# Optimization experiments

Hardware: AMD Instinct MI355X
Metric: run time of the kernel (lower is better)

Reference implementation:

```python
import jax, jax.numpy as jnp
import numpy as np

N_NODES = 100000
N_EDGES = 1600000
N_FEAT, N_HID, N_CLS = 256, 64, 16


def setup_inputs() -> dict:
    key = jax.random.key(0)
    ks = jax.random.split(key, 8)
    x = jax.random.normal(ks[0], (N_NODES, N_FEAT), dtype=jnp.float32)
    adj_row = jax.random.randint(ks[1], (N_EDGES,), 0, N_NODES, dtype=jnp.int32)
    adj_col = jax.random.randint(ks[2], (N_EDGES,), 0, N_NODES, dtype=jnp.int32)
    adj_vals = jax.random.uniform(ks[3], (N_EDGES,), dtype=jnp.float32)
    W1 = jax.random.normal(ks[4], (N_FEAT, N_HID), dtype=jnp.float32) * 0.05
    b1 = jnp.zeros((N_HID,), dtype=jnp.float32)
    W2 = jax.random.normal(ks[5], (N_HID, N_CLS), dtype=jnp.float32) * 0.05
    b2 = jnp.zeros((N_CLS,), dtype=jnp.float32)
    return {"x": x, "adj_row": adj_row, "adj_col": adj_col, "adj_vals": adj_vals,
            "W1": W1, "b1": b1, "W2": W2, "b2": b2}


def _spmm(row, col, vals, h):
    # sparse [N,N] @ dense [N,D]: gather source rows, scale, scatter-add to dest rows
    msgs = vals[:, None] * h[col]                       # [E, D]
    return jax.ops.segment_sum(msgs, row, num_segments=N_NODES)


def reference(x, adj_row, adj_col, adj_vals, W1, b1, W2, b2):
    # layer 1: linear -> spmm -> relu  (dropout is identity at inference)
    h = _spmm(adj_row, adj_col, adj_vals, x @ W1 + b1)  # [N, n_hidden]
    h = jax.nn.relu(h)
    # layer 2: linear -> spmm -> log_softmax
    out = _spmm(adj_row, adj_col, adj_vals, h @ W2 + b2)  # [N, n_class]
    return jax.nn.log_softmax(out, axis=1)
```

## Files before the change

### kernel.cpp

```cpp
#include <hip/hip_runtime.h>

#define N_NODES 100000
#define N_EDGES 1600000
#define N_FEAT  256
#define N_HID   64
#define N_CLS   16
#define NB      391
#define CHUNK   8192
#define NSCAT   196
#define NGEMM1  1563
#define NHIST   256

typedef unsigned short bfraw;
typedef unsigned int uint32;

typedef __attribute__((ext_vector_type(8))) short  bf16x8;
typedef __attribute__((ext_vector_type(4))) float  f32x4;

__device__ __forceinline__ bfraw f2bf(float f) {
    union { float f; unsigned int i; } v; v.f = f;
    unsigned int x = v.i;
    return (bfraw)((x + 0x7FFFu + ((x >> 16) & 1u)) >> 16);
}

__device__ __forceinline__ float bf_lo(uint32 g) { return __uint_as_float(g << 16); }
__device__ __forceinline__ float bf_hi(uint32 g) { return __uint_as_float(g & 0xFFFF0000u); }

__global__ __launch_bounds__(256) void w1cvt_hist_k(const float* __restrict__ W1,
                                                    bfraw* __restrict__ w1f,
                                                    const int* __restrict__ rowi,
                                                    int* __restrict__ part) {
    __shared__ int lh[NB];
    if (blockIdx.x < 64) {
        int i = blockIdx.x * 256 + threadIdx.x;
        int k = i >> 6, n = i & 63;
        w1f[((size_t)((k >> 3) * 64 + n) << 3) + (k & 7)] = f2bf(W1[i]);
        return;
    }
    const int hb = blockIdx.x - 64;
    for (int i = threadIdx.x; i < NB; i += 256) lh[i] = 0;
    __syncthreads();
    const int4* r4p = (const int4*)rowi;
    for (int i = hb * 256 + threadIdx.x; i < N_EDGES / 4; i += 256 * 256) {
        int4 r = r4p[i];
        atomicAdd(&lh[r.x >> 8], 1);
        atomicAdd(&lh[r.y >> 8], 1);
        atomicAdd(&lh[r.z >> 8], 1);
        atomicAdd(&lh[r.w >> 8], 1);
    }
    __syncthreads();
    for (int i = threadIdx.x; i < NB; i += 256)
        part[hb * NB + i] = lh[i];
}

__global__ __launch_bounds__(512) void bscan_k(const int* __restrict__ part,
                                               int* __restrict__ bbase,
                                               int* __restrict__ gcur,
                                               int* __restrict__ rp) {
    __shared__ int s[512];
    int t = threadIdx.x;
    int v = 0;
    if (t < NB) {
        #pragma unroll 8
        for (int hb = 0; hb < NHIST; ++hb) v += part[hb * NB + t];
    }
    s[t] = v;
    __syncthreads();
    #pragma unroll
    for (int off = 1; off < 512; off <<= 1) {
        int x = (t >= off) ? s[t - off] : 0;
        __syncthreads();
        s[t] += x;
        __syncthreads();
    }
    if (t <= NB) {
        int b = s[t] - v;
        bbase[t] = b;
        if (t < NB) gcur[t] = b;
    }
    if (t == 0) rp[N_NODES] = N_EDGES;
}

__global__ __launch_bounds__(256) void scatter_gemm1_k(const int* __restrict__ rowi,
                                                       const int* __restrict__ coli,
                                                       const float* __restrict__ vals,
                                                       int* __restrict__ gcur,
                                                       int2* __restrict__ edges,
                                                       const float* __restrict__ x,
                                                       const bfraw* __restrict__ w1f,
                                                       const float* __restrict__ b1,
                                                       bfraw* __restrict__ h0) {
    __shared__ int lh[NB];
    __shared__ int lb[NB];
    const int t = threadIdx.x;

    if (blockIdx.x < NSCAT) {
        const int e0   = blockIdx.x * CHUNK;
        const bool full = (e0 + CHUNK <= N_EDGES);
        for (int i = t; i < NB; i += 256) lh[i] = 0;
        __syncthreads();

        int4 r4[8];
        if (full) {
            const int4* rp4 = (const int4*)(rowi + e0);
            #pragma unroll
            for (int u = 0; u < 8; ++u) r4[u] = rp4[t + u * 256];
            #pragma unroll
            for (int u = 0; u < 8; ++u) {
                atomicAdd(&lh[r4[u].x >> 8], 1);
                atomicAdd(&lh[r4[u].y >> 8], 1);
                atomicAdd(&lh[r4[u].z >> 8], 1);
                atomicAdd(&lh[r4[u].w >> 8], 1);
            }
        } else {
            for (int j = t; j < CHUNK; j += 256) {
                int e = e0 + j;
                if (e < N_EDGES) atomicAdd(&lh[rowi[e] >> 8], 1);
            }
        }
        __syncthreads();
        for (int i = t; i < NB; i += 256) {
            int c = lh[i];
            lb[i] = c ? atomicAdd(&gcur[i], c) : 0;
            lh[i] = 0;
        }
        __syncthreads();
        if (full) {
            const int4*   cp4 = (const int4*)(coli + e0);
            const float4* vp4 = (const float4*)(vals + e0);
            #pragma unroll
            for (int u = 0; u < 8; ++u) {
                int4   c4 = cp4[t + u * 256];
                float4 v4 = vp4[t + u * 256];
                int r, b, rk;
                r = r4[u].x; b = r >> 8; rk = atomicAdd(&lh[b], 1);
                edges[lb[b] + rk] = make_int2(c4.x | ((r & 255) << 17), __float_as_int(v4.x));
                r = r4[u].y; b = r >> 8; rk = atomicAdd(&lh[b], 1);
                edges[lb[b] + rk] = make_int2(c4.y | ((r & 255) << 17), __float_as_int(v4.y));
                r = r4[u].z; b = r >> 8; rk = atomicAdd(&lh[b], 1);
                edges[lb[b] + rk] = make_int2(c4.z | ((r & 255) << 17), __float_as_int(v4.z));
                r = r4[u].w; b = r >> 8; rk = atomicAdd(&lh[b], 1);
                edges[lb[b] + rk] = make_int2(c4.w | ((r & 255) << 17), __float_as_int(v4.w));
            }
        } else {
            for (int j = t; j < CHUNK; j += 256) {
                int e = e0 + j;
                if (e < N_EDGES) {
                    int r  = rowi[e];
                    int b  = r >> 8;
                    int rk = atomicAdd(&lh[b], 1);
                    edges[lb[b] + rk] = make_int2(coli[e] | ((r & 255) << 17),
                                                  __float_as_int(vals[e]));
                }
            }
        }
        return;
    }

    const int bg   = blockIdx.x - NSCAT;
    const int w    = t >> 6;
    const int lane = t & 63;
    const int q    = lane >> 4;
    const int m    = lane & 15;

    const int row  = bg * 64 + w * 16 + m;
    const int srow = row < N_NODES ? row : N_NODES - 1;
    const float* xp = x + (size_t)srow * N_FEAT + q * 8;
    const bf16x8* w1v = (const bf16x8*)w1f;

    float4 x0[8], x1[8];
    #pragma unroll
    for (int s = 0; s < 8; ++s) {
        x0[s] = *(const float4*)(xp + s * 32);
        x1[s] = *(const float4*)(xp + s * 32 + 4);
    }

    f32x4 acc[4];
    #pragma unroll
    for (int nt = 0; nt < 4; ++nt) acc[nt] = (f32x4){0.f, 0.f, 0.f, 0.f};

    #pragma unroll
    for (int s = 0; s < 8; ++s) {
        bf16x8 af;
        af[0] = (short)f2bf(x0[s].x); af[1] = (short)f2bf(x0[s].y);
        af[2] = (short)f2bf(x0[s].z); af[3] = (short)f2bf(x0[s].w);
        af[4] = (short)f2bf(x1[s].x); af[5] = (short)f2bf(x1[s].y);
        af[6] = (short)f2bf(x1[s].z); af[7] = (short)f2bf(x1[s].w);
        const int g = s * 4 + q;
        #pragma unroll
        for (int nt = 0; nt < 4; ++nt) {
            bf16x8 bf_ = w1v[g * 64 + nt * 16 + m];
            acc[nt] = __builtin_amdgcn_mfma_f32_16x16x32_bf16(af, bf_, acc[nt], 0, 0, 0);
        }
    }

    float bb[4];
    #pragma unroll
    for (int nt = 0; nt < 4; ++nt) bb[nt] = b1[nt * 16 + m];

    const int orow0 = bg * 64 + w * 16 + q * 4;
    #pragma unroll
    for (int r = 0; r < 4; ++r) {
        int orow = orow0 + r;
        if (orow < N_NODES) {
            bfraw* op = h0 + (size_t)orow * N_HID + m;
            #pragma unroll
            for (int nt = 0; nt < 4; ++nt)
                op[nt * 16] = f2bf(acc[nt][r] + bb[nt]);
        }
    }
}

__global__ __launch_bounds__(256) void sort_k(const int* __restrict__ bbase,
                                              const int2* __restrict__ edges,
                                              int2* __restrict__ edges2,
                                              int* __restrict__ rp) {
    __shared__ int cnt[256];
    __shared__ int pos[256];
    const int t   = threadIdx.x;
    const int b   = blockIdx.x;
    const int beg = bbase[b];
    const int end = bbase[b + 1];

    cnt[t] = 0;
    __syncthreads();
    {
        int i = beg + t;
        for (; i + 768 < end; i += 1024) {
            int2 a = edges[i], c = edges[i + 256], d = edges[i + 512], e = edges[i + 768];
            atomicAdd(&cnt[(a.x >> 17) & 255], 1);
            atomicAdd(&cnt[(c.x >> 17) & 255], 1);
            atomicAdd(&cnt[(d.x >> 17) & 255], 1);
            atomicAdd(&cnt[(e.x >> 17) & 255], 1);
        }
        for (; i < end; i += 256)
            atomicAdd(&cnt[(edges[i].x >> 17) & 255], 1);
    }
    __syncthreads();

    int v = cnt[t];
    pos[t] = v;
    __syncthreads();
    #pragma unroll
    for (int off = 1; off < 256; off <<= 1) {
        int y = (t >= off) ? pos[t - off] : 0;
        __syncthreads();
        pos[t] += y;
        __syncthreads();
    }
    int excl = pos[t] - v;

    int row = (b << 8) + t;
    if (row < N_NODES) rp[row] = beg + excl;
    __syncthreads();
    pos[t] = excl;
    __syncthreads();

    {
        int i = beg + t;
        for (; i + 768 < end; i += 1024) {
            int2 E0 = edges[i], E1 = edges[i + 256], E2 = edges[i + 512], E3 = edges[i + 768];
            int r0 = (E0.x >> 17) & 255, r1 = (E1.x >> 17) & 255;
            int r2 = (E2.x >> 17) & 255, r3 = (E3.x >> 17) & 255;
            int k0 = atomicAdd(&pos[r0], 1);
            int k1 = atomicAdd(&pos[r1], 1);
            int k2 = atomicAdd(&pos[r2], 1);
            int k3 = atomicAdd(&pos[r3], 1);
            edges2[beg + k0] = make_int2(E0.x & 0x1FFFF, E0.y);
            edges2[beg + k1] = make_int2(E1.x & 0x1FFFF, E1.y);
            edges2[beg + k2] = make_int2(E2.x & 0x1FFFF, E2.y);
            edges2[beg + k3] = make_int2(E3.x & 0x1FFFF, E3.y);
        }
        for (; i < end; i += 256) {
            int2 E = edges[i];
            int r  = (E.x >> 17) & 255;
            int rk = atomicAdd(&pos[r], 1);
            edges2[beg + rk] = make_int2(E.x & 0x1FFFF, E.y);
        }
    }
}

__global__ __launch_bounds__(256) void spmm1_fused3_k(const int* __restrict__ rp,
                                                      const int2* __restrict__ edges2,
                                                      const uint32* __restrict__ h0p,
                                                      const float* __restrict__ W2,
                                                      const float* __restrict__ b2,
                                                      float* __restrict__ h2) {
    __shared__ float Hs[16][68];
    __shared__ float Ws[64 * 16];
    __shared__ float bs[16];
    const int t = threadIdx.x;
    *(float4*)&Ws[t * 4] = ((const float4*)W2)[t];
    if (t < 16) bs[t] = b2[t];

    const int g16 = t >> 4;
    const int l   = t & 15;
    const int row = blockIdx.x * 16 + g16;
    const int beg = rp[row];
    const int end = rp[row + 1];

    const uint2* h0v = (const uint2*)h0p;

    float a0 = 0.f, a1 = 0.f, a2 = 0.f, a3 = 0.f;
    int i = beg;
    for (; i + 8 <= end; i += 8) {
        int2 E[8];
        #pragma unroll
        for (int u = 0; u < 8; ++u) E[u] = edges2[i + u];
        uint2 q[8];
        #pragma unroll
        for (int u = 0; u < 8; ++u) q[u] = h0v[(size_t)E[u].x * 16 + l];
        #pragma unroll
        for (int u = 0; u < 8; ++u) {
            float v = __int_as_float(E[u].y);
            a0 += v * bf_lo(q[u].x); a1 += v * bf_hi(q[u].x);
            a2 += v * bf_lo(q[u].y); a3 += v * bf_hi(q[u].y);
        }
    }
    for (; i + 4 <= end; i += 4) {
        int2 E[4];
        #pragma unroll
        for (int u = 0; u < 4; ++u) E[u] = edges2[i + u];
        uint2 q[4];
        #pragma unroll
        for (int u = 0; u < 4; ++u) q[u] = h0v[(size_t)E[u].x * 16 + l];
        #pragma unroll
        for (int u = 0; u < 4; ++u) {
            float v = __int_as_float(E[u].y);
            a0 += v * bf_lo(q[u].x); a1 += v * bf_hi(q[u].x);
            a2 += v * bf_lo(q[u].y); a3 += v * bf_hi(q[u].y);
        }
    }
    for (; i < end; ++i) {
        int2 E = edges2[i];
        uint2 q = h0v[(size_t)E.x * 16 + l];
        float v = __int_as_float(E.y);
        a0 += v * bf_lo(q.x); a1 += v * bf_hi(q.x);
        a2 += v * bf_lo(q.y); a3 += v * bf_hi(q.y);
    }

    *(float4*)&Hs[g16][4 * l] = make_float4(fmaxf(a0, 0.f), fmaxf(a1, 0.f),
                                            fmaxf(a2, 0.f), fmaxf(a3, 0.f));
    __syncthreads();

    const int r = t >> 4;
    const int c = t & 15;
    float a = bs[c];
    #pragma unroll
    for (int k = 0; k < 64; ++k)
        a += Hs[r][k] * Ws[k * 16 + c];
    h2[(size_t)(blockIdx.x * 16 + r) * N_CLS + c] = a;
}

__global__ __launch_bounds__(256) void spmm2_lsm_k(const int* __restrict__ rp,
                                                   const int2* __restrict__ edges2,
                                                   const float* __restrict__ h2,
                                                   float* __restrict__ outp) {
    const int l   = threadIdx.x & 7;
    const int row = blockIdx.x * 32 + (threadIdx.x >> 3);
    const int beg = rp[row];
    const int end = rp[row + 1];
    const float2* h2v = (const float2*)h2;

    float a0 = 0.f, a1 = 0.f;
    int i = beg;
    for (; i + 8 <= end; i += 8) {
        int2 e[8];
        #pragma unroll
        for (int u = 0; u < 8; ++u) e[u] = edges2[i + u];
        float2 g[8];
        #pragma unroll
        for (int u = 0; u < 8; ++u) g[u] = h2v[(size_t)e[u].x * 8 + l];
        #pragma unroll
        for (int u = 0; u < 8; ++u) {
            float v = __int_as_float(e[u].y);
            a0 += v * g[u].x; a1 += v * g[u].y;
        }
    }
    for (; i + 4 <= end; i += 4) {
        int2 e[4];
        #pragma unroll
        for (int u = 0; u < 4; ++u) e[u] = edges2[i + u];
        float2 g[4];
        #pragma unroll
        for (int u = 0; u < 4; ++u) g[u] = h2v[(size_t)e[u].x * 8 + l];
        #pragma unroll
        for (int u = 0; u < 4; ++u) {
            float v = __int_as_float(e[u].y);
            a0 += v * g[u].x; a1 += v * g[u].y;
        }
    }
    for (; i < end; ++i) {
        int2 e = edges2[i];
        float2 g = h2v[(size_t)e.x * 8 + l];
        float v = __int_as_float(e.y);
        a0 += v * g.x; a1 += v * g.y;
    }

    float m = fmaxf(a0, a1);
    #pragma unroll
    for (int off = 4; off; off >>= 1) m = fmaxf(m, __shfl_xor(m, off, 8));
    float ex = expf(a0 - m) + expf(a1 - m);
    float s = ex;
    #pragma unroll
    for (int off = 4; off; off >>= 1) s += __shfl_xor(s, off, 8);
    float ls = logf(s);
    *(float2*)(outp + (size_t)row * N_CLS + 2 * l) =
        make_float2(a0 - m - ls, a1 - m - ls);
}

extern "C" void kernel_launch(void* const* d_in, const int* in_sizes, int n_in,
                              void* d_out, int out_size, void* d_ws, size_t ws_size,
                              hipStream_t stream) {
    const float* x        = (const float*)d_in[0];
    const int*   adj_row  = (const int*)d_in[1];
    const int*   adj_col  = (const int*)d_in[2];
    const float* adj_vals = (const float*)d_in[3];
    const float* W1       = (const float*)d_in[4];
    const float* b1       = (const float*)d_in[5];
    const float* W2       = (const float*)d_in[6];
    const float* b2       = (const float*)d_in[7];
    float*       out      = (float*)d_out;

    const size_t H0_BYTES = (size_t)N_NODES * N_HID * sizeof(bfraw);
    const size_t H2_BYTES = (size_t)N_NODES * N_CLS * sizeof(float);
    const size_t E_BYTES  = (size_t)N_EDGES * sizeof(int2);
    bfraw* h0     = (bfraw*)d_ws;
    float* h2     = (float*)((char*)d_ws + H0_BYTES);
    int2*  edges  = (int2*)((char*)h2 + H2_BYTES);
    int2*  edges2 = (int2*)((char*)edges + E_BYTES);
    int*   bbase  = (int*)((char*)edges2 + E_BYTES);
    int*   gcur   = bbase + NB + 1;
    int*   rp     = gcur + NB;
    bfraw* w1f    = (bfraw*)(rp + N_NODES + 1);
    int*   part   = (int*)(w1f + 16384);

    w1cvt_hist_k<<<320, 256, 0, stream>>>(W1, w1f, adj_row, part);
    bscan_k<<<1, 512, 0, stream>>>(part, bbase, gcur, rp);
    scatter_gemm1_k<<<NSCAT + NGEMM1, 256, 0, stream>>>(adj_row, adj_col, adj_vals,
                                                        gcur, edges,
                                                        x, w1f, b1, h0);
    sort_k<<<NB, 256, 0, stream>>>(bbase, edges, edges2, rp);

    spmm1_fused3_k<<<N_NODES / 16, 256, 0, stream>>>(rp, edges2, (const uint32*)h0,
                                                     W2, b2, h2);

    spmm2_lsm_k<<<N_NODES / 32, 256, 0, stream>>>(rp, edges2, h2, out);
}
```

Baseline: 280.6 us.

## Move GEMM1 from scatter kernel into sort kernel and widen scatter blocks

The dense x@W1 GEMM blocks are moved from the scatter launch into the per-bucket sort launch, so GEMM1 runs alongside the sort phase instead of the scatter phase. The scatter becomes its own kernel with 1024-thread blocks, each handling the same 8192-edge chunk with fewer elements per thread. The GEMM inner loop now loads x per step rather than preloading all 16 float4s, which lowers register pressure. The aim is to balance work across the two launches and give better occupancy, at the cost of changing how much overlap each phase gets.

```diff
diff --git a/kernel.cpp b/kernel.cpp
--- a/kernel.cpp
+++ b/kernel.cpp
@@ -81,83 +81,152 @@
     if (t == 0) rp[N_NODES] = N_EDGES;
 }
 
-__global__ __launch_bounds__(256) void scatter_gemm1_k(const int* __restrict__ rowi,
-                                                       const int* __restrict__ coli,
-                                                       const float* __restrict__ vals,
-                                                       int* __restrict__ gcur,
-                                                       int2* __restrict__ edges,
-                                                       const float* __restrict__ x,
-                                                       const bfraw* __restrict__ w1f,
-                                                       const float* __restrict__ b1,
-                                                       bfraw* __restrict__ h0) {
+__global__ __launch_bounds__(1024) void scatter_k(const int* __restrict__ rowi,
+                                                  const int* __restrict__ coli,
+                                                  const float* __restrict__ vals,
+                                                  int* __restrict__ gcur,
+                                                  int2* __restrict__ edges) {
     __shared__ int lh[NB];
     __shared__ int lb[NB];
+    const int t    = threadIdx.x;
+    const int e0   = blockIdx.x * CHUNK;
+    const bool full = (e0 + CHUNK <= N_EDGES);
+    for (int i = t; i < NB; i += 1024) lh[i] = 0;
+    __syncthreads();
+
+    int4 r4[2];
+    if (full) {
+        const int4* rp4 = (const int4*)(rowi + e0);
+        #pragma unroll
+        for (int u = 0; u < 2; ++u) r4[u] = rp4[t + u * 1024];
+        #pragma unroll
+        for (int u = 0; u < 2; ++u) {
+            atomicAdd(&lh[r4[u].x >> 8], 1);
+            atomicAdd(&lh[r4[u].y >> 8], 1);
+            atomicAdd(&lh[r4[u].z >> 8], 1);
+            atomicAdd(&lh[r4[u].w >> 8], 1);
+        }
+    } else {
+        for (int j = t; j < CHUNK; j += 1024) {
+            int e = e0 + j;
+            if (e < N_EDGES) atomicAdd(&lh[rowi[e] >> 8], 1);
+        }
+    }
+    __syncthreads();
+    for (int i = t; i < NB; i += 1024) {
+        int c = lh[i];
+        lb[i] = c ? atomicAdd(&gcur[i], c) : 0;
+        lh[i] = 0;
+    }
+    __syncthreads();
+    if (full) {
+        const int4*   cp4 = (const int4*)(coli + e0);
+        const float4* vp4 = (const float4*)(vals + e0);
+        #pragma unroll
+        for (int u = 0; u < 2; ++u) {
+            int4   c4 = cp4[t + u * 1024];
+            float4 v4 = vp4[t + u * 1024];
+            int r, b, rk;
+            r = r4[u].x; b = r >> 8; rk = atomicAdd(&lh[b], 1);
+            edges[lb[b] + rk] = make_int2(c4.x | ((r & 255) << 17), __float_as_int(v4.x));
+            r = r4[u].y; b = r >> 8; rk = atomicAdd(&lh[b], 1);
+            edges[lb[b] + rk] = make_int2(c4.y | ((r & 255) << 17), __float_as_int(v4.y));
+            r = r4[u].z; b = r >> 8; rk = atomicAdd(&lh[b], 1);
+            edges[lb[b] + rk] = make_int2(c4.z | ((r & 255) << 17), __float_as_int(v4.z));
+            r = r4[u].w; b = r >> 8; rk = atomicAdd(&lh[b], 1);
+            edges[lb[b] + rk] = make_int2(c4.w | ((r & 255) << 17), __float_as_int(v4.w));
+        }
+    } else {
+        for (int j = t; j < CHUNK; j += 1024) {
+            int e = e0 + j;
+            if (e < N_EDGES) {
+                int r  = rowi[e];
+                int b  = r >> 8;
+                int rk = atomicAdd(&lh[b], 1);
+                edges[lb[b] + rk] = make_int2(coli[e] | ((r & 255) << 17),
+                                              __float_as_int(vals[e]));
+            }
+        }
+    }
+}
+
+__global__ __launch_bounds__(256) void sort_gemm1_k(const int* __restrict__ bbase,
+                                                    const int2* __restrict__ edges,
+                                                    int2* __restrict__ edges2,
+                                                    int* __restrict__ rp,
+                                                    const float* __restrict__ x,
+                                                    const bfraw* __restrict__ w1f,
+                                                    const float* __restrict__ b1,
+                                                    bfraw* __restrict__ h0) {
+    __shared__ int cnt[256];
+    __shared__ int pos[256];
     const int t = threadIdx.x;
 
-    if (blockIdx.x < NSCAT) {
-        const int e0   = blockIdx.x * CHUNK;
-        const bool full = (e0 + CHUNK <= N_EDGES);
-        for (int i = t; i < NB; i += 256) lh[i] = 0;
-        __syncthreads();
-
-        int4 r4[8];
-        if (full) {
-            const int4* rp4 = (const int4*)(rowi + e0);
-            #pragma unroll
-            for (int u = 0; u < 8; ++u) r4[u] = rp4[t + u * 256];
-            #pragma unroll
-            for (int u = 0; u < 8; ++u) {
-                atomicAdd(&lh[r4[u].x >> 8], 1);
-                atomicAdd(&lh[r4[u].y >> 8], 1);
-                atomicAdd(&lh[r4[u].z >> 8], 1);
-                atomicAdd(&lh[r4[u].w >> 8], 1);
+    if (blockIdx.x < NB) {
+        const int b   = blockIdx.x;
+        const int beg = bbase[b];
+        const int end = bbase[b + 1];
+
+        cnt[t] = 0;
+        __syncthreads();
+        {
+            int i = beg + t;
+            for (; i + 768 < end; i += 1024) {
+                int2 a = edges[i], c = edges[i + 256], d = edges[i + 512], e = edges[i + 768];
+                atomicAdd(&cnt[(a.x >> 17) & 255], 1);
+                atomicAdd(&cnt[(c.x >> 17) & 255], 1);
+                atomicAdd(&cnt[(d.x >> 17) & 255], 1);
+                atomicAdd(&cnt[(e.x >> 17) & 255], 1);
             }
-        } else {
-            for (int j = t; j < CHUNK; j += 256) {
-                int e = e0 + j;
-                if (e < N_EDGES) atomicAdd(&lh[rowi[e] >> 8], 1);
+            for (; i < end; i += 256)
+                atomicAdd(&cnt[(edges[i].x >> 17) & 255], 1);
+        }
+        __syncthreads();
+
+        int v = cnt[t];
+        pos[t] = v;
+        __syncthreads();
+        #pragma unroll
+        for (int off = 1; off < 256; off <<= 1) {
+            int y = (t >= off) ? pos[t - off] : 0;
+            __syncthreads();
+            pos[t] += y;
+            __syncthreads();
+        }
+        int excl = pos[t] - v;
+
+        int row = (b << 8) + t;
+        if (row < N_NODES) rp[row] = beg + excl;
+        __syncthreads();
+        pos[t] = excl;
+        __syncthreads();
+
+        {
+            int i = beg + t;
+            for (; i + 768 < end; i += 1024) {
+                int2 E0 = edges[i], E1 = edges[i + 256], E2 = edges[i + 512], E3 = edges[i + 768];
+                int r0 = (E0.x >> 17) & 255, r1 = (E1.x >> 17) & 255;
+                int r2 = (E2.x >> 17) & 255, r3 = (E3.x >> 17) & 255;
+                int k0 = atomicAdd(&pos[r0], 1);
+                int k1 = atomicAdd(&pos[r1], 1);
+                int k2 = atomicAdd(&pos[r2], 1);
+                int k3 = atomicAdd(&pos[r3], 1);
+                edges2[beg + k0] = make_int2(E0.x & 0x1FFFF, E0.y);
+                edges2[beg + k1] = make_int2(E1.x & 0x1FFFF, E1.y);
+                edges2[beg + k2] = make_int2(E2.x & 0x1FFFF, E2.y);
+                edges2[beg + k3] = make_int2(E3.x & 0x1FFFF, E3.y);
             }
-        }
-        __syncthreads();
-        for (int i = t; i < NB; i += 256) {
-            int c = lh[i];
-            lb[i] = c ? atomicAdd(&gcur[i], c) : 0;
-            lh[i] = 0;
-        }
-        __syncthreads();
-        if (full) {
-            const int4*   cp4 = (const int4*)(coli + e0);
-            const float4* vp4 = (const float4*)(vals + e0);
-            #pragma unroll
-            for (int u = 0; u < 8; ++u) {
-                int4   c4 = cp4[t + u * 256];
-                float4 v4 = vp4[t + u * 256];
-                int r, b, rk;
-                r = r4[u].x; b = r >> 8; rk = atomicAdd(&lh[b], 1);
-                edges[lb[b] + rk] = make_int2(c4.x | ((r & 255) << 17), __float_as_int(v4.x));
-                r = r4[u].y; b = r >> 8; rk = atomicAdd(&lh[b], 1);
-                edges[lb[b] + rk] = make_int2(c4.y | ((r & 255) << 17), __float_as_int(v4.y));
-                r = r4[u].z; b = r >> 8; rk = atomicAdd(&lh[b], 1);
-                edges[lb[b] + rk] = make_int2(c4.z | ((r & 255) << 17), __float_as_int(v4.z));
-                r = r4[u].w; b = r >> 8; rk = atomicAdd(&lh[b], 1);
-                edges[lb[b] + rk] = make_int2(c4.w | ((r & 255) << 17), __float_as_int(v4.w));
+            for (; i < end; i += 256) {
+                int2 E = edges[i];
+                int r  = (E.x >> 17) & 255;
+                int rk = atomicAdd(&pos[r], 1);
+                edges2[beg + rk] = make_int2(E.x & 0x1FFFF, E.y);
             }
-        } else {
-            for (int j = t; j < CHUNK; j += 256) {
-                int e = e0 + j;
-                if (e < N_EDGES) {
-                    int r  = rowi[e];
-                    int b  = r >> 8;
-                    int rk = atomicAdd(&lh[b], 1);
-                    edges[lb[b] + rk] = make_int2(coli[e] | ((r & 255) << 17),
-                                                  __float_as_int(vals[e]));
-                }
-            }
         }
         return;
     }
 
-    const int bg   = blockIdx.x - NSCAT;
+    const int bg   = blockIdx.x - NB;
     const int w    = t >> 6;
     const int lane = t & 63;
     const int q    = lane >> 4;
@@ -168,24 +237,19 @@
     const float* xp = x + (size_t)srow * N_FEAT + q * 8;
     const bf16x8* w1v = (const bf16x8*)w1f;
 
-    float4 x0[8], x1[8];
+    f32x4 acc[4];
+    #pragma unroll
+    for (int nt = 0; nt < 4; ++nt) acc[nt] = (f32x4){0.f, 0.f, 0.f, 0.f};
+
     #pragma unroll
     for (int s = 0; s < 8; ++s) {
-        x0[s] = *(const float4*)(xp + s * 32);
-        x1[s] = *(const float4*)(xp + s * 32 + 4);
-    }
-
-    f32x4 acc[4];
-    #pragma unroll
-    for (int nt = 0; nt < 4; ++nt) acc[nt] = (f32x4){0.f, 0.f, 0.f, 0.f};
-
-    #pragma unroll
-    for (int s = 0; s < 8; ++s) {
+        float4 a0 = *(const float4*)(xp + s * 32);
+        float4 a1 = *(const float4*)(xp + s * 32 + 4);
         bf16x8 af;
-        af[0] = (short)f2bf(x0[s].x); af[1] = (short)f2bf(x0[s].y);
-        af[2] = (short)f2bf(x0[s].z); af[3] = (short)f2bf(x0[s].w);
-        af[4] = (short)f2bf(x1[s].x); af[5] = (short)f2bf(x1[s].y);
-        af[6] = (short)f2bf(x1[s].z); af[7] = (short)f2bf(x1[s].w);
+        af[0] = (short)f2bf(a0.x); af[1] = (short)f2bf(a0.y);
+        af[2] = (short)f2bf(a0.z); af[3] = (short)f2bf(a0.w);
+        af[4] = (short)f2bf(a1.x); af[5] = (short)f2bf(a1.y);
+        af[6] = (short)f2bf(a1.z); af[7] = (short)f2bf(a1.w);
         const int g = s * 4 + q;
         #pragma unroll
         for (int nt = 0; nt < 4; ++nt) {
@@ -207,75 +271,6 @@
             #pragma unroll
             for (int nt = 0; nt < 4; ++nt)
                 op[nt * 16] = f2bf(acc[nt][r] + bb[nt]);
-        }
-    }
-}
-
-__global__ __launch_bounds__(256) void sort_k(const int* __restrict__ bbase,
-                                              const int2* __restrict__ edges,
-                                              int2* __restrict__ edges2,
-                                              int* __restrict__ rp) {
-    __shared__ int cnt[256];
-    __shared__ int pos[256];
-    const int t   = threadIdx.x;
-    const int b   = blockIdx.x;
-    const int beg = bbase[b];
-    const int end = bbase[b + 1];
-
-    cnt[t] = 0;
-    __syncthreads();
-    {
-        int i = beg + t;
-        for (; i + 768 < end; i += 1024) {
-            int2 a = edges[i], c = edges[i + 256], d = edges[i + 512], e = edges[i + 768];
-            atomicAdd(&cnt[(a.x >> 17) & 255], 1);
-            atomicAdd(&cnt[(c.x >> 17) & 255], 1);
-            atomicAdd(&cnt[(d.x >> 17) & 255], 1);
-            atomicAdd(&cnt[(e.x >> 17) & 255], 1);
-        }
-        for (; i < end; i += 256)
-            atomicAdd(&cnt[(edges[i].x >> 17) & 255], 1);
-    }
-    __syncthreads();
-
-    int v = cnt[t];
-    pos[t] = v;
-    __syncthreads();
-    #pragma unroll
-    for (int off = 1; off < 256; off <<= 1) {
-        int y = (t >= off) ? pos[t - off] : 0;
-        __syncthreads();
-        pos[t] += y;
-        __syncthreads();
-    }
-    int excl = pos[t] - v;
-
-    int row = (b << 8) + t;
-    if (row < N_NODES) rp[row] = beg + excl;
-    __syncthreads();
-    pos[t] = excl;
-    __syncthreads();
-
-    {
-        int i = beg + t;
-        for (; i + 768 < end; i += 1024) {
-            int2 E0 = edges[i], E1 = edges[i + 256], E2 = edges[i + 512], E3 = edges[i + 768];
-            int r0 = (E0.x >> 17) & 255, r1 = (E1.x >> 17) & 255;
-            int r2 = (E2.x >> 17) & 255, r3 = (E3.x >> 17) & 255;
-            int k0 = atomicAdd(&pos[r0], 1);
-            int k1 = atomicAdd(&pos[r1], 1);
-            int k2 = atomicAdd(&pos[r2], 1);
-            int k3 = atomicAdd(&pos[r3], 1);
-            edges2[beg + k0] = make_int2(E0.x & 0x1FFFF, E0.y);
-            edges2[beg + k1] = make_int2(E1.x & 0x1FFFF, E1.y);
-            edges2[beg + k2] = make_int2(E2.x & 0x1FFFF, E2.y);
-            edges2[beg + k3] = make_int2(E3.x & 0x1FFFF, E3.y);
-        }
-        for (; i < end; i += 256) {
-            int2 E = edges[i];
-            int r  = (E.x >> 17) & 255;
-            int rk = atomicAdd(&pos[r], 1);
-            edges2[beg + rk] = make_int2(E.x & 0x1FFFF, E.y);
         }
     }
 }
@@ -437,10 +432,9 @@
 
     w1cvt_hist_k<<<320, 256, 0, stream>>>(W1, w1f, adj_row, part);
     bscan_k<<<1, 512, 0, stream>>>(part, bbase, gcur, rp);
-    scatter_gemm1_k<<<NSCAT + NGEMM1, 256, 0, stream>>>(adj_row, adj_col, adj_vals,
-                                                        gcur, edges,
-                                                        x, w1f, b1, h0);
-    sort_k<<<NB, 256, 0, stream>>>(bbase, edges, edges2, rp);
+    scatter_k<<<NSCAT, 1024, 0, stream>>>(adj_row, adj_col, adj_vals, gcur, edges);
+    sort_gemm1_k<<<NB + NGEMM1, 256, 0, stream>>>(bbase, edges, edges2, rp,
+                                                  x, w1f, b1, h0);
 
     spmm1_fused3_k<<<N_NODES / 16, 256, 0, stream>>>(rp, edges2, (const uint32*)h0,
                                                      W2, b2, h2);
```

Result: no change. 281.6 us (+0.4%).
